# Kernel tuning notes

Hardware: AMD Instinct MI355X
Metric: run time of the kernel (lower is better)

The kernel has to match this reference:

```python
import jax, jax.numpy as jnp
import numpy as np

N_NODES = 100000
N_EDGES = 3200000
PERIODS = 12
C_IN, C_OUT, F_OUT = 1, 4, 12


def setup_inputs() -> dict:
    key = jax.random.key(0)
    ks = jax.random.split(key, 20)
    s = 0.1
    return {
        "x": jax.random.normal(ks[0], (N_NODES, C_IN, PERIODS), dtype=jnp.float32),
        "edge_index": jax.random.randint(ks[1], (2, N_EDGES), 0, N_NODES, dtype=jnp.int32),
        "conv_z_w": s * jax.random.normal(ks[2], (C_IN, C_OUT), dtype=jnp.float32),
        "conv_z_b": s * jax.random.normal(ks[3], (C_OUT,), dtype=jnp.float32),
        "lin_z_w": s * jax.random.normal(ks[4], (2 * C_OUT, C_OUT), dtype=jnp.float32),
        "lin_z_b": s * jax.random.normal(ks[5], (C_OUT,), dtype=jnp.float32),
        "conv_r_w": s * jax.random.normal(ks[6], (C_IN, C_OUT), dtype=jnp.float32),
        "conv_r_b": s * jax.random.normal(ks[7], (C_OUT,), dtype=jnp.float32),
        "lin_r_w": s * jax.random.normal(ks[8], (2 * C_OUT, C_OUT), dtype=jnp.float32),
        "lin_r_b": s * jax.random.normal(ks[9], (C_OUT,), dtype=jnp.float32),
        "conv_h_w": s * jax.random.normal(ks[10], (C_IN, C_OUT), dtype=jnp.float32),
        "conv_h_b": s * jax.random.normal(ks[11], (C_OUT,), dtype=jnp.float32),
        "lin_h_w": s * jax.random.normal(ks[12], (2 * C_OUT, C_OUT), dtype=jnp.float32),
        "lin_h_b": s * jax.random.normal(ks[13], (C_OUT,), dtype=jnp.float32),
        "att": jax.random.normal(ks[14], (PERIODS,), dtype=jnp.float32),
        "out_w": s * jax.random.normal(ks[15], (C_OUT, F_OUT), dtype=jnp.float32),
        "out_b": s * jax.random.normal(ks[16], (F_OUT,), dtype=jnp.float32),
        "f": 12,
    }


def reference(x, edge_index, conv_z_w, conv_z_b, lin_z_w, lin_z_b,
              conv_r_w, conv_r_b, lin_r_w, lin_r_b,
              conv_h_w, conv_h_b, lin_h_w, lin_h_b,
              att, out_w, out_b, f):
    N, _, P = x.shape
    loops = jnp.arange(N, dtype=edge_index.dtype)
    src = jnp.concatenate([edge_index[0], loops])  # self loops, fill=1
    dst = jnp.concatenate([edge_index[1], loops])
    deg = jax.ops.segment_sum(jnp.ones_like(src, dtype=x.dtype), dst, num_segments=N)
    dinv = jnp.where(deg > 0, jax.lax.rsqrt(deg), 0.0)
    norm = dinv[src] * dinv[dst]  # [E+N] symmetric GCN normalization

    def gcn(xt, W, b):
        xw = xt @ W  # [N, C_OUT]
        msg = xw[src] * norm[:, None]
        return jax.ops.segment_sum(msg, dst, num_segments=N) + b

    H0 = jnp.zeros((N, conv_z_w.shape[1]), dtype=x.dtype)

    def tgcn_step(xt):  # xt: [N, C_IN]; A3TGCN does not carry H across periods
        z = jax.nn.sigmoid(jnp.concatenate([gcn(xt, conv_z_w, conv_z_b), H0], 1) @ lin_z_w + lin_z_b)
        r = jax.nn.sigmoid(jnp.concatenate([gcn(xt, conv_r_w, conv_r_b), H0], 1) @ lin_r_w + lin_r_b)
        h_t = jnp.tanh(jnp.concatenate([gcn(xt, conv_h_w, conv_h_b), r * H0], 1) @ lin_h_w + lin_h_b)
        return z * H0 + (1.0 - z) * h_t

    xs = jnp.transpose(x, (2, 0, 1))  # [P, N, C_IN]
    Hs = jax.vmap(tgcn_step)(xs)  # [P, N, C_OUT]
    probs = jax.nn.softmax(att)
    H_accum = jnp.einsum('p,pnd->nd', probs, Hs)  # attention over periods
    out = H_accum @ out_w + out_b  # [N, 12]
    return out[:, :f]
```

## Files before the change

### kernel.cpp

```cpp
#include <hip/hip_runtime.h>
#include <hip/hip_fp16.h>
#include <math.h>


#define PERIODS 12
#define BSZ     256
#define BSH     8
#define STRIDE  9216
#define SRCBITS 17
#define SMASK   ((1 << SRCBITS) - 1)
#define CH      8192
#define NT      1024
#define ACCW    7
#define BIAS_F  262144.f

struct Consts {
    float az[4], cz[4], ah[4], ch[4], probs[PERIODS];
};

typedef float vf2 __attribute__((ext_vector_type(2)));

__device__ __forceinline__ float dec1_manual(unsigned b) {
    unsigned e = (b >> 3) & 15u, m = b & 7u;
    float v = e ? __uint_as_float(((e + 120u) << 23) | (m << 20))
                : (float)m * 0.001953125f;
    return (b & 0x80u) ? -v : v;
}

__device__ __forceinline__ void dec4(unsigned u, float* o) {
#if __has_builtin(__builtin_amdgcn_cvt_pk_f32_fp8)
    vf2 lo = __builtin_amdgcn_cvt_pk_f32_fp8((int)u, false);
    vf2 hi = __builtin_amdgcn_cvt_pk_f32_fp8((int)u, true);
    o[0] = lo.x; o[1] = lo.y; o[2] = hi.x; o[3] = hi.y;
#else
    o[0] = dec1_manual(u & 255u);
    o[1] = dec1_manual((u >> 8) & 255u);
    o[2] = dec1_manual((u >> 16) & 255u);
    o[3] = dec1_manual(u >> 24);
#endif
}

__device__ __forceinline__ unsigned enc1_manual(float x) {
    unsigned s = (__float_as_uint(x) >> 24) & 0x80u;
    float a = fabsf(x);
    if (!(a > 0.f)) return s;
    a = fminf(a, 448.f);
    int eb = (int)(__float_as_uint(a) >> 23) - 127;
    int e = eb < -6 ? -6 : eb;
    float q = rintf(a * exp2f((float)(3 - e)));
    if (q >= 16.f) { e++; q = rintf(a * exp2f((float)(3 - e))); }
    if (e > 8) return s | 0x7Eu;
    int m = (int)q;
    unsigned ee, mm;
    if (m >= 8) { ee = (unsigned)(e + 7); mm = (unsigned)(m - 8); }
    else        { ee = 0u; mm = (unsigned)m; }
    return s | (ee << 3) | mm;
}

__device__ __forceinline__ unsigned pk4(float a, float b, float c, float d) {
#if __has_builtin(__builtin_amdgcn_cvt_pk_fp8_f32)
    int v = __builtin_amdgcn_cvt_pk_fp8_f32(a, b, 0, false);
    v = __builtin_amdgcn_cvt_pk_fp8_f32(c, d, v, true);
    return (unsigned)v;
#else
    return enc1_manual(a) | (enc1_manual(b) << 8) |
           (enc1_manual(c) << 16) | (enc1_manual(d) << 24);
#endif
}


__global__ __launch_bounds__(512) void k_setup(const float* conv_z_w, const float* conv_z_b,
                        const float* lin_z_w, const float* lin_z_b,
                        const float* conv_h_w, const float* conv_h_b,
                        const float* lin_h_w, const float* lin_h_b,
                        const float* att, Consts* C, int* gcur, int NB)
{
    int t = threadIdx.x;
    for (int i = t; i < NB; i += 512) gcur[i] = 0;
    if (t == 0) {
        for (int c = 0; c < 4; ++c) {
            float az = 0.f, cz = 0.f, ah = 0.f, ch = 0.f;
            for (int k = 0; k < 4; ++k) {
                az += conv_z_w[k] * lin_z_w[k * 4 + c];
                cz += conv_z_b[k] * lin_z_w[k * 4 + c];
                ah += conv_h_w[k] * lin_h_w[k * 4 + c];
                ch += conv_h_b[k] * lin_h_w[k * 4 + c];
            }
            C->az[c] = az; C->cz[c] = cz + lin_z_b[c];
            C->ah[c] = ah; C->ch[c] = ch + lin_h_b[c];
        }
        float m = att[0];
        for (int p = 1; p < PERIODS; ++p) m = fmaxf(m, att[p]);
        float e[PERIODS]; float s = 0.f;
        for (int p = 0; p < PERIODS; ++p) { e[p] = expf(att[p] - m); s += e[p]; }
        for (int p = 0; p < PERIODS; ++p) C->probs[p] = e[p] / s;
    }
}

__global__ __launch_bounds__(NT, 4) void k_binA(const int* __restrict__ ei,
                                                int* __restrict__ gcur,
                                                int* __restrict__ binned, int E) {
    __shared__ int hist[512];
    __shared__ int scn[512];
    __shared__ int gdel[512];
    __shared__ int sv[CH];
    __shared__ int sa[CH];
    int t = threadIdx.x;
    if (t < 512) hist[t] = 0;
    __syncthreads();
    int base = blockIdx.x * CH;
    int lim = min(E - base, CH);
    int rs[CH / NT], rd[CH / NT];
    #pragma unroll
    for (int k = 0; k < CH / NT; ++k) {
        int i = t + k * NT;
        if (i < lim) {
            rs[k] = ei[base + i];
            rd[k] = ei[E + base + i];
            atomicAdd(&hist[rd[k] >> BSH], 1);
        }
    }
    __syncthreads();
    int v = 0;
    if (t < 512) { v = hist[t]; scn[t] = v; }
    __syncthreads();
    for (int off = 1; off < 512; off <<= 1) {
        int tmp = 0;
        if (t < 512 && t >= off) tmp = scn[t - off];
        __syncthreads();
        if (t < 512) scn[t] += tmp;
        __syncthreads();
    }
    if (t < 512) {
        int excl = scn[t] - v;
        int g = (v > 0) ? atomicAdd(&gcur[t], v) : 0;
        gdel[t] = t * STRIDE + g - excl;
        hist[t] = excl;
    }
    __syncthreads();
    #pragma unroll
    for (int k = 0; k < CH / NT; ++k) {
        int i = t + k * NT;
        if (i < lim) {
            int s = rs[k];
            int d = rd[k];
            int b = d >> BSH;
            int pos = atomicAdd(&hist[b], 1);
            sv[pos] = ((d & (BSZ - 1)) << SRCBITS) | s;
            sa[pos] = gdel[b] + pos;
        }
    }
    __syncthreads();
    for (int j = t; j < lim; j += NT)
        binned[sa[j]] = sv[j];
}

__global__ __launch_bounds__(NT, 4) void k_degprep(const int* __restrict__ binned,
                                                   const int* __restrict__ gcur,
                                                   const float* __restrict__ x,
                                                   int* __restrict__ deg,
                                                   float* __restrict__ dinv,
                                                   uint4* __restrict__ xs8, int N) {
    __shared__ int hist[BSZ];
    int b = blockIdx.x, t = threadIdx.x;
    if (t < BSZ) hist[t] = 0;
    __syncthreads();
    int cnt = gcur[b];
    const int* bb = binned + b * STRIDE;
    for (int i = t; i < cnt; i += NT)
        atomicAdd(&hist[bb[i] >> SRCBITS], 1);
    __syncthreads();
    if (t >= BSZ) return;
    int n = (b << BSH) + t;
    if (n >= N) return;
    int dg = hist[t];
    deg[n] = dg;
    float di = rsqrtf((float)dg + 1.0f);
    dinv[n] = di;
    const float4* xv = (const float4*)(x + (size_t)n * PERIODS);
    float4 v0 = xv[0], v1 = xv[1], v2 = xv[2];
    uint4 r;
    r.x = pk4(v0.x * di, v0.y * di, v0.z * di, v0.w * di);
    r.y = pk4(v1.x * di, v1.y * di, v1.z * di, v1.w * di);
    r.z = pk4(v2.x * di, v2.y * di, v2.z * di, v2.w * di);
    r.w = 0;
    xs8[n] = r;
}

__device__ __forceinline__ void scat(unsigned long long* acc, int d, uint4 r) {
    float f[PERIODS];
    dec4(r.x, f + 0); dec4(r.y, f + 4); dec4(r.z, f + 8);
    int base = d * ACCW;
    #pragma unroll
    for (int k = 0; k < 6; ++k) {
        unsigned lo = (unsigned)__float2int_rn(fmaf(f[k],     512.f, BIAS_F));
        unsigned hi = (unsigned)__float2int_rn(fmaf(f[k + 6], 512.f, BIAS_F));
        atomicAdd(&acc[base + k], ((unsigned long long)hi << 32) | (unsigned long long)lo);
    }
}

__global__ __launch_bounds__(NT, 4) void k_agg(const int* __restrict__ binned,
                                               const int* __restrict__ gcur,
                                               const int* __restrict__ deg,
                                               const float* __restrict__ dinv,
                                               const uint4* __restrict__ xs8,
                                               const Consts* __restrict__ C,
                                               const float* __restrict__ out_w,
                                               const float* __restrict__ out_b,
                                               float* __restrict__ out, int N) {
    __shared__ unsigned long long acc[BSZ * ACCW];
    int b = blockIdx.x, t = threadIdx.x;
    for (int i = t; i < BSZ * ACCW; i += NT) acc[i] = 0ull;
    __syncthreads();
    int cnt = gcur[b];
    const int* bb = binned + b * STRIDE;
    int i = t;
    for (; i + 3 * NT < cnt; i += 4 * NT) {
        int p0 = bb[i];
        int p1 = bb[i + NT];
        int p2 = bb[i + 2 * NT];
        int p3 = bb[i + 3 * NT];
        uint4 r0 = xs8[p0 & SMASK];
        uint4 r1 = xs8[p1 & SMASK];
        uint4 r2 = xs8[p2 & SMASK];
        uint4 r3 = xs8[p3 & SMASK];
        scat(acc, p0 >> SRCBITS, r0);
        scat(acc, p1 >> SRCBITS, r1);
        scat(acc, p2 >> SRCBITS, r2);
        scat(acc, p3 >> SRCBITS, r3);
    }
    for (; i < cnt; i += NT) {
        int pv = bb[i];
        uint4 r = xs8[pv & SMASK];
        scat(acc, pv >> SRCBITS, r);
    }
    __syncthreads();

    if (t >= BSZ) return;
    int n = (b << BSH) + t;
    if (n >= N) return;

    int corr = deg[n] << 18;
    float a[PERIODS];
    {
        float f[PERIODS];
        uint4 r = xs8[n];
        dec4(r.x, f + 0); dec4(r.y, f + 4); dec4(r.z, f + 8);
        #pragma unroll
        for (int k = 0; k < 6; ++k) {
            unsigned long long u = acc[t * ACCW + k];
            int lo = (int)(unsigned)(u & 0xFFFFFFFFull) - corr;
            int hi = (int)(unsigned)(u >> 32) - corr;
            a[k]     = (float)lo * 0.001953125f + f[k];
            a[k + 6] = (float)hi * 0.001953125f + f[k + 6];
        }
    }

    float di = dinv[n];
    float hacc[4] = {0.f, 0.f, 0.f, 0.f};
    #pragma unroll
    for (int p = 0; p < PERIODS; ++p) {
        float ap = di * a[p];
        float pr = C->probs[p];
        #pragma unroll
        for (int c = 0; c < 4; ++c) {
            float zz = 1.f / (1.f + __expf(-(ap * C->az[c] + C->cz[c])));
            float hh = tanhf(ap * C->ah[c] + C->ch[c]);
            hacc[c] += pr * (1.f - zz) * hh;
        }
    }
    float o[PERIODS];
    #pragma unroll
    for (int f = 0; f < PERIODS; ++f) {
        float v = out_b[f];
        #pragma unroll
        for (int c = 0; c < 4; ++c) v += hacc[c] * out_w[c * PERIODS + f];
        o[f] = v;
    }
    float4* ov = (float4*)(out + (size_t)n * PERIODS);
    ov[0] = make_float4(o[0], o[1], o[2],  o[3]);
    ov[1] = make_float4(o[4], o[5], o[6],  o[7]);
    ov[2] = make_float4(o[8], o[9], o[10], o[11]);
}

extern "C" void kernel_launch(void* const* d_in, const int* in_sizes, int n_in,
                              void* d_out, int out_size, void* d_ws, size_t ws_size,
                              hipStream_t stream) {
    const float* x        = (const float*)d_in[0];
    const int*   ei       = (const int*)d_in[1];
    const float* conv_z_w = (const float*)d_in[2];
    const float* conv_z_b = (const float*)d_in[3];
    const float* lin_z_w  = (const float*)d_in[4];
    const float* lin_z_b  = (const float*)d_in[5];
    const float* conv_h_w = (const float*)d_in[10];
    const float* conv_h_b = (const float*)d_in[11];
    const float* lin_h_w  = (const float*)d_in[12];
    const float* lin_h_b  = (const float*)d_in[13];
    const float* att      = (const float*)d_in[14];
    const float* out_w    = (const float*)d_in[15];
    const float* out_b    = (const float*)d_in[16];
    float* out = (float*)d_out;

    const int N  = in_sizes[0] / PERIODS;
    const int E  = in_sizes[1] / 2;
    const int NB = (N + BSZ - 1) / BSZ;
    const int gA = (E + CH - 1) / CH;

    char* ws = (char*)d_ws;
    size_t off = 0;
    Consts* consts = (Consts*)(ws + off);  off += (sizeof(Consts) + 255) & ~255ull;
    int*    gcur   = (int*)(ws + off);     off += ((size_t)NB * 4 + 255) & ~255ull;
    int*    deg    = (int*)(ws + off);     off += ((size_t)N * 4 + 255) & ~255ull;
    float*  dinv   = (float*)(ws + off);   off += ((size_t)N * 4 + 255) & ~255ull;
    uint4*  xs8    = (uint4*)(ws + off);   off += ((size_t)(N + 256) * 16 + 255) & ~255ull;
    int*    binned = (int*)(ws + off);     off += ((size_t)NB * STRIDE * 4 + 255) & ~255ull;
    (void)ws_size; (void)n_in; (void)out_size;

    k_setup<<<1, 512, 0, stream>>>(conv_z_w, conv_z_b, lin_z_w, lin_z_b,
                                   conv_h_w, conv_h_b, lin_h_w, lin_h_b, att,
                                   consts, gcur, NB);
    k_binA<<<gA, NT, 0, stream>>>(ei, gcur, binned, E);
    k_degprep<<<NB, NT, 0, stream>>>(binned, gcur, x, deg, dinv, xs8, N);
    k_agg<<<NB, NT, 0, stream>>>(binned, gcur, deg, dinv, xs8, consts,
                                 out_w, out_b, out, N);
}
```

Measured before the change: 160.0 us.

## Split per-bin aggregation into sliced partial-accumulate kernel plus merge kernel

```diff
diff --git a/kernel.cpp b/kernel.cpp
--- a/kernel.cpp
+++ b/kernel.cpp
@@ -6,7 +6,9 @@
 #define PERIODS 12
 #define BSZ     256
 #define BSH     8
-#define STRIDE  9216
+#define STRIDE  13312
+#define SLICE   3328
+#define NSLICE  4
 #define SRCBITS 17
 #define SMASK   ((1 << SRCBITS) - 1)
 #define CH      8192
@@ -99,7 +101,7 @@
 
 __global__ __launch_bounds__(NT, 4) void k_binA(const int* __restrict__ ei,
                                                 int* __restrict__ gcur,
-                                                int* __restrict__ binned, int E) {
+                                                int* __restrict__ binned, int E, int N) {
     __shared__ int hist[512];
     __shared__ int scn[512];
     __shared__ int gdel[512];
@@ -131,10 +133,13 @@
         if (t < 512) scn[t] += tmp;
         __syncthreads();
     }
+    int gbase = 0, vp = 0;
     if (t < 512) {
         int excl = scn[t] - v;
-        int g = (v > 0) ? atomicAdd(&gcur[t], v) : 0;
-        gdel[t] = t * STRIDE + g - excl;
+        vp = (v + 15) & ~15;
+        int g = (vp > 0) ? atomicAdd(&gcur[t], vp) : 0;
+        gbase = t * STRIDE + g;
+        gdel[t] = gbase - excl;
         hist[t] = excl;
     }
     __syncthreads();
@@ -153,6 +158,10 @@
     __syncthreads();
     for (int j = t; j < lim; j += NT)
         binned[sa[j]] = sv[j];
+    if (t < 512) {
+        for (int j = v; j < vp; ++j)
+            binned[gbase + j] = N;
+    }
 }
 
 __global__ __launch_bounds__(NT, 4) void k_degprep(const int* __restrict__ binned,
@@ -167,9 +176,12 @@
     __syncthreads();
     int cnt = gcur[b];
     const int* bb = binned + b * STRIDE;
-    for (int i = t; i < cnt; i += NT)
-        atomicAdd(&hist[bb[i] >> SRCBITS], 1);
-    __syncthreads();
+    for (int i = t; i < cnt; i += NT) {
+        int pv = bb[i];
+        if ((pv & SMASK) < N) atomicAdd(&hist[pv >> SRCBITS], 1);
+    }
+    __syncthreads();
+    if (b == 0 && t == 0) xs8[N] = make_uint4(0, 0, 0, 0);
     if (t >= BSZ) return;
     int n = (b << BSH) + t;
     if (n >= N) return;
@@ -199,8 +211,44 @@
     }
 }
 
-__global__ __launch_bounds__(NT, 4) void k_agg(const int* __restrict__ binned,
-                                               const int* __restrict__ gcur,
+__global__ __launch_bounds__(512) void k_aggp(const int* __restrict__ binned,
+                                              const int* __restrict__ gcur,
+                                              const uint4* __restrict__ xs8,
+                                              unsigned long long* __restrict__ pacc,
+                                              int N) {
+    __shared__ unsigned long long acc[BSZ * ACCW];
+    int b = blockIdx.x >> 2, s = blockIdx.x & 3;
+    int t = threadIdx.x;
+    for (int i = t; i < BSZ * ACCW; i += 512) acc[i] = 0ull;
+    __syncthreads();
+    int cnt = gcur[b];
+    int end = min(cnt, (s + 1) * SLICE);
+    const int* bb = binned + b * STRIDE;
+    int i = s * SLICE + t;
+    for (; i + 512 < end; i += 1024) {
+        int p0 = bb[i];
+        int p1 = bb[i + 512];
+        int s0 = p0 & SMASK, s1 = p1 & SMASK;
+        uint4 r0 = xs8[s0];
+        uint4 r1 = xs8[s1];
+        if (s0 < N) scat(acc, p0 >> SRCBITS, r0);
+        if (s1 < N) scat(acc, p1 >> SRCBITS, r1);
+    }
+    for (; i < end; i += 512) {
+        int pv = bb[i];
+        int sv = pv & SMASK;
+        uint4 r = xs8[sv];
+        if (sv < N) scat(acc, pv >> SRCBITS, r);
+    }
+    __syncthreads();
+    unsigned long long* pb = pacc + (size_t)(b * NSLICE + s) * (BSZ * 6);
+    for (int j = t; j < BSZ * 6; j += 512) {
+        int node = j / 6, k = j - node * 6;
+        pb[j] = acc[node * ACCW + k];
+    }
+}
+
+__global__ __launch_bounds__(256) void k_merge(const unsigned long long* __restrict__ pacc,
                                                const int* __restrict__ deg,
                                                const float* __restrict__ dinv,
                                                const uint4* __restrict__ xs8,
@@ -208,37 +256,17 @@
                                                const float* __restrict__ out_w,
                                                const float* __restrict__ out_b,
                                                float* __restrict__ out, int N) {
-    __shared__ unsigned long long acc[BSZ * ACCW];
     int b = blockIdx.x, t = threadIdx.x;
-    for (int i = t; i < BSZ * ACCW; i += NT) acc[i] = 0ull;
-    __syncthreads();
-    int cnt = gcur[b];
-    const int* bb = binned + b * STRIDE;
-    int i = t;
-    for (; i + 3 * NT < cnt; i += 4 * NT) {
-        int p0 = bb[i];
-        int p1 = bb[i + NT];
-        int p2 = bb[i + 2 * NT];
-        int p3 = bb[i + 3 * NT];
-        uint4 r0 = xs8[p0 & SMASK];
-        uint4 r1 = xs8[p1 & SMASK];
-        uint4 r2 = xs8[p2 & SMASK];
-        uint4 r3 = xs8[p3 & SMASK];
-        scat(acc, p0 >> SRCBITS, r0);
-        scat(acc, p1 >> SRCBITS, r1);
-        scat(acc, p2 >> SRCBITS, r2);
-        scat(acc, p3 >> SRCBITS, r3);
-    }
-    for (; i < cnt; i += NT) {
-        int pv = bb[i];
-        uint4 r = xs8[pv & SMASK];
-        scat(acc, pv >> SRCBITS, r);
-    }
-    __syncthreads();
-
-    if (t >= BSZ) return;
     int n = (b << BSH) + t;
     if (n >= N) return;
+
+    unsigned long long sum[6] = {0ull, 0ull, 0ull, 0ull, 0ull, 0ull};
+    const unsigned long long* pb = pacc + (size_t)b * NSLICE * (BSZ * 6) + t * 6;
+    #pragma unroll
+    for (int s = 0; s < NSLICE; ++s) {
+        #pragma unroll
+        for (int k = 0; k < 6; ++k) sum[k] += pb[s * (BSZ * 6) + k];
+    }
 
     int corr = deg[n] << 18;
     float a[PERIODS];
@@ -248,9 +276,8 @@
         dec4(r.x, f + 0); dec4(r.y, f + 4); dec4(r.z, f + 8);
         #pragma unroll
         for (int k = 0; k < 6; ++k) {
-            unsigned long long u = acc[t * ACCW + k];
-            int lo = (int)(unsigned)(u & 0xFFFFFFFFull) - corr;
-            int hi = (int)(unsigned)(u >> 32) - corr;
+            int lo = (int)(unsigned)(sum[k] & 0xFFFFFFFFull) - corr;
+            int hi = (int)(unsigned)(sum[k] >> 32) - corr;
             a[k]     = (float)lo * 0.001953125f + f[k];
             a[k + 6] = (float)hi * 0.001953125f + f[k + 6];
         }
@@ -314,13 +341,16 @@
     float*  dinv   = (float*)(ws + off);   off += ((size_t)N * 4 + 255) & ~255ull;
     uint4*  xs8    = (uint4*)(ws + off);   off += ((size_t)(N + 256) * 16 + 255) & ~255ull;
     int*    binned = (int*)(ws + off);     off += ((size_t)NB * STRIDE * 4 + 255) & ~255ull;
+    unsigned long long* pacc = (unsigned long long*)(ws + off);
+    off += ((size_t)NB * NSLICE * BSZ * 6 * 8 + 255) & ~255ull;
     (void)ws_size; (void)n_in; (void)out_size;
 
     k_setup<<<1, 512, 0, stream>>>(conv_z_w, conv_z_b, lin_z_w, lin_z_b,
                                    conv_h_w, conv_h_b, lin_h_w, lin_h_b, att,
                                    consts, gcur, NB);
-    k_binA<<<gA, NT, 0, stream>>>(ei, gcur, binned, E);
+    k_binA<<<gA, NT, 0, stream>>>(ei, gcur, binned, E, N);
     k_degprep<<<NB, NT, 0, stream>>>(binned, gcur, x, deg, dinv, xs8, N);
-    k_agg<<<NB, NT, 0, stream>>>(binned, gcur, deg, dinv, xs8, consts,
-                                 out_w, out_b, out, N);
-}
+    k_aggp<<<NB * NSLICE, 512, 0, stream>>>(binned, gcur, xs8, pacc, N);
+    k_merge<<<NB, 256, 0, stream>>>(pacc, deg, dinv, xs8, consts,
+                                    out_w, out_b, out, N);
+}
```

Result: no change. 163.2 us (+2.0%).

## Replicate shared accumulators 4x, pad bins to 16, fold setup into aggregation

Applied to the files above, without the earlier changes.

```diff
diff --git a/kernel.cpp b/kernel.cpp
--- a/kernel.cpp
+++ b/kernel.cpp
@@ -6,17 +6,14 @@
 #define PERIODS 12
 #define BSZ     256
 #define BSH     8
-#define STRIDE  9216
+#define STRIDE  13312
 #define SRCBITS 17
 #define SMASK   ((1 << SRCBITS) - 1)
 #define CH      8192
 #define NT      1024
 #define ACCW    7
+#define ACPY    1799
 #define BIAS_F  262144.f
-
-struct Consts {
-    float az[4], cz[4], ah[4], ch[4], probs[PERIODS];
-};
 
 typedef float vf2 __attribute__((ext_vector_type(2)));
 
@@ -69,37 +66,9 @@
 }
 
 
-__global__ __launch_bounds__(512) void k_setup(const float* conv_z_w, const float* conv_z_b,
-                        const float* lin_z_w, const float* lin_z_b,
-                        const float* conv_h_w, const float* conv_h_b,
-                        const float* lin_h_w, const float* lin_h_b,
-                        const float* att, Consts* C, int* gcur, int NB)
-{
-    int t = threadIdx.x;
-    for (int i = t; i < NB; i += 512) gcur[i] = 0;
-    if (t == 0) {
-        for (int c = 0; c < 4; ++c) {
-            float az = 0.f, cz = 0.f, ah = 0.f, ch = 0.f;
-            for (int k = 0; k < 4; ++k) {
-                az += conv_z_w[k] * lin_z_w[k * 4 + c];
-                cz += conv_z_b[k] * lin_z_w[k * 4 + c];
-                ah += conv_h_w[k] * lin_h_w[k * 4 + c];
-                ch += conv_h_b[k] * lin_h_w[k * 4 + c];
-            }
-            C->az[c] = az; C->cz[c] = cz + lin_z_b[c];
-            C->ah[c] = ah; C->ch[c] = ch + lin_h_b[c];
-        }
-        float m = att[0];
-        for (int p = 1; p < PERIODS; ++p) m = fmaxf(m, att[p]);
-        float e[PERIODS]; float s = 0.f;
-        for (int p = 0; p < PERIODS; ++p) { e[p] = expf(att[p] - m); s += e[p]; }
-        for (int p = 0; p < PERIODS; ++p) C->probs[p] = e[p] / s;
-    }
-}
-
 __global__ __launch_bounds__(NT, 4) void k_binA(const int* __restrict__ ei,
                                                 int* __restrict__ gcur,
-                                                int* __restrict__ binned, int E) {
+                                                int* __restrict__ binned, int E, int N) {
     __shared__ int hist[512];
     __shared__ int scn[512];
     __shared__ int gdel[512];
@@ -131,10 +100,13 @@
         if (t < 512) scn[t] += tmp;
         __syncthreads();
     }
+    int gbase = 0, vp = 0;
     if (t < 512) {
         int excl = scn[t] - v;
-        int g = (v > 0) ? atomicAdd(&gcur[t], v) : 0;
-        gdel[t] = t * STRIDE + g - excl;
+        vp = (v + 15) & ~15;
+        int g = (vp > 0) ? atomicAdd(&gcur[t], vp) : 0;
+        gbase = t * STRIDE + g;
+        gdel[t] = gbase - excl;
         hist[t] = excl;
     }
     __syncthreads();
@@ -153,6 +125,10 @@
     __syncthreads();
     for (int j = t; j < lim; j += NT)
         binned[sa[j]] = sv[j];
+    if (t < 512) {
+        for (int j = v; j < vp; ++j)
+            binned[gbase + j] = N;
+    }
 }
 
 __global__ __launch_bounds__(NT, 4) void k_degprep(const int* __restrict__ binned,
@@ -161,19 +137,23 @@
                                                    int* __restrict__ deg,
                                                    float* __restrict__ dinv,
                                                    uint4* __restrict__ xs8, int N) {
-    __shared__ int hist[BSZ];
+    __shared__ int hist[4 * 257];
     int b = blockIdx.x, t = threadIdx.x;
-    if (t < BSZ) hist[t] = 0;
+    for (int i = t; i < 4 * 257; i += NT) hist[i] = 0;
     __syncthreads();
     int cnt = gcur[b];
     const int* bb = binned + b * STRIDE;
-    for (int i = t; i < cnt; i += NT)
-        atomicAdd(&hist[bb[i] >> SRCBITS], 1);
-    __syncthreads();
+    int cpy = (t & 3) * 257;
+    for (int i = t; i < cnt; i += NT) {
+        int pv = bb[i];
+        if ((pv & SMASK) < N) atomicAdd(&hist[cpy + (pv >> SRCBITS)], 1);
+    }
+    __syncthreads();
+    if (b == 0 && t == 0) xs8[N] = make_uint4(0, 0, 0, 0);
     if (t >= BSZ) return;
     int n = (b << BSH) + t;
     if (n >= N) return;
-    int dg = hist[t];
+    int dg = hist[t] + hist[257 + t] + hist[514 + t] + hist[771 + t];
     deg[n] = dg;
     float di = rsqrtf((float)dg + 1.0f);
     dinv[n] = di;
@@ -187,31 +167,40 @@
     xs8[n] = r;
 }
 
-__device__ __forceinline__ void scat(unsigned long long* acc, int d, uint4 r) {
+__device__ __forceinline__ void scat(unsigned long long* accb, int d, uint4 r) {
     float f[PERIODS];
     dec4(r.x, f + 0); dec4(r.y, f + 4); dec4(r.z, f + 8);
-    int base = d * ACCW;
+    int ba = d * ACCW;
     #pragma unroll
     for (int k = 0; k < 6; ++k) {
         unsigned lo = (unsigned)__float2int_rn(fmaf(f[k],     512.f, BIAS_F));
         unsigned hi = (unsigned)__float2int_rn(fmaf(f[k + 6], 512.f, BIAS_F));
-        atomicAdd(&acc[base + k], ((unsigned long long)hi << 32) | (unsigned long long)lo);
-    }
-}
-
-__global__ __launch_bounds__(NT, 4) void k_agg(const int* __restrict__ binned,
+        atomicAdd(&accb[ba + k], ((unsigned long long)hi << 32) | (unsigned long long)lo);
+    }
+}
+
+__global__ __launch_bounds__(NT, 2) void k_agg(const int* __restrict__ binned,
                                                const int* __restrict__ gcur,
                                                const int* __restrict__ deg,
                                                const float* __restrict__ dinv,
                                                const uint4* __restrict__ xs8,
-                                               const Consts* __restrict__ C,
+                                               const float* __restrict__ conv_z_w,
+                                               const float* __restrict__ conv_z_b,
+                                               const float* __restrict__ lin_z_w,
+                                               const float* __restrict__ lin_z_b,
+                                               const float* __restrict__ conv_h_w,
+                                               const float* __restrict__ conv_h_b,
+                                               const float* __restrict__ lin_h_w,
+                                               const float* __restrict__ lin_h_b,
+                                               const float* __restrict__ att,
                                                const float* __restrict__ out_w,
                                                const float* __restrict__ out_b,
                                                float* __restrict__ out, int N) {
-    __shared__ unsigned long long acc[BSZ * ACCW];
+    __shared__ unsigned long long acc[4 * ACPY];
     int b = blockIdx.x, t = threadIdx.x;
-    for (int i = t; i < BSZ * ACCW; i += NT) acc[i] = 0ull;
-    __syncthreads();
+    for (int i = t; i < 4 * ACPY; i += NT) acc[i] = 0ull;
+    __syncthreads();
+    unsigned long long* accb = acc + (t & 3) * ACPY;
     int cnt = gcur[b];
     const int* bb = binned + b * STRIDE;
     int i = t;
@@ -220,25 +209,54 @@
         int p1 = bb[i + NT];
         int p2 = bb[i + 2 * NT];
         int p3 = bb[i + 3 * NT];
-        uint4 r0 = xs8[p0 & SMASK];
-        uint4 r1 = xs8[p1 & SMASK];
-        uint4 r2 = xs8[p2 & SMASK];
-        uint4 r3 = xs8[p3 & SMASK];
-        scat(acc, p0 >> SRCBITS, r0);
-        scat(acc, p1 >> SRCBITS, r1);
-        scat(acc, p2 >> SRCBITS, r2);
-        scat(acc, p3 >> SRCBITS, r3);
+        int s0 = p0 & SMASK, s1 = p1 & SMASK, s2 = p2 & SMASK, s3 = p3 & SMASK;
+        uint4 r0 = xs8[s0];
+        uint4 r1 = xs8[s1];
+        uint4 r2 = xs8[s2];
+        uint4 r3 = xs8[s3];
+        if (s0 < N) scat(accb, p0 >> SRCBITS, r0);
+        if (s1 < N) scat(accb, p1 >> SRCBITS, r1);
+        if (s2 < N) scat(accb, p2 >> SRCBITS, r2);
+        if (s3 < N) scat(accb, p3 >> SRCBITS, r3);
     }
     for (; i < cnt; i += NT) {
         int pv = bb[i];
-        uint4 r = xs8[pv & SMASK];
-        scat(acc, pv >> SRCBITS, r);
+        int sv = pv & SMASK;
+        uint4 r = xs8[sv];
+        if (sv < N) scat(accb, pv >> SRCBITS, r);
     }
     __syncthreads();
 
     if (t >= BSZ) return;
     int n = (b << BSH) + t;
     if (n >= N) return;
+
+    float az[4], cz[4], ah[4], ch[4];
+    #pragma unroll
+    for (int c = 0; c < 4; ++c) {
+        float a1 = 0.f, c1 = 0.f, a2 = 0.f, c2 = 0.f;
+        #pragma unroll
+        for (int k = 0; k < 4; ++k) {
+            a1 += conv_z_w[k] * lin_z_w[k * 4 + c];
+            c1 += conv_z_b[k] * lin_z_w[k * 4 + c];
+            a2 += conv_h_w[k] * lin_h_w[k * 4 + c];
+            c2 += conv_h_b[k] * lin_h_w[k * 4 + c];
+        }
+        az[c] = a1; cz[c] = c1 + lin_z_b[c];
+        ah[c] = a2; ch[c] = c2 + lin_h_b[c];
+    }
+    float probs[PERIODS];
+    {
+        float m = att[0];
+        #pragma unroll
+        for (int p = 1; p < PERIODS; ++p) m = fmaxf(m, att[p]);
+        float ssum = 0.f;
+        #pragma unroll
+        for (int p = 0; p < PERIODS; ++p) { probs[p] = expf(att[p] - m); ssum += probs[p]; }
+        float inv = 1.f / ssum;
+        #pragma unroll
+        for (int p = 0; p < PERIODS; ++p) probs[p] *= inv;
+    }
 
     int corr = deg[n] << 18;
     float a[PERIODS];
@@ -246,9 +264,11 @@
         float f[PERIODS];
         uint4 r = xs8[n];
         dec4(r.x, f + 0); dec4(r.y, f + 4); dec4(r.z, f + 8);
+        int ba = t * ACCW;
         #pragma unroll
         for (int k = 0; k < 6; ++k) {
-            unsigned long long u = acc[t * ACCW + k];
+            unsigned long long u = acc[ba + k] + acc[ACPY + ba + k]
+                                 + acc[2 * ACPY + ba + k] + acc[3 * ACPY + ba + k];
             int lo = (int)(unsigned)(u & 0xFFFFFFFFull) - corr;
             int hi = (int)(unsigned)(u >> 32) - corr;
             a[k]     = (float)lo * 0.001953125f + f[k];
@@ -261,11 +281,11 @@
     #pragma unroll
     for (int p = 0; p < PERIODS; ++p) {
         float ap = di * a[p];
-        float pr = C->probs[p];
+        float pr = probs[p];
         #pragma unroll
         for (int c = 0; c < 4; ++c) {
-            float zz = 1.f / (1.f + __expf(-(ap * C->az[c] + C->cz[c])));
-            float hh = tanhf(ap * C->ah[c] + C->ch[c]);
+            float zz = 1.f / (1.f + __expf(-(ap * az[c] + cz[c])));
+            float hh = tanhf(ap * ah[c] + ch[c]);
             hacc[c] += pr * (1.f - zz) * hh;
         }
     }
@@ -308,7 +328,6 @@
 
     char* ws = (char*)d_ws;
     size_t off = 0;
-    Consts* consts = (Consts*)(ws + off);  off += (sizeof(Consts) + 255) & ~255ull;
     int*    gcur   = (int*)(ws + off);     off += ((size_t)NB * 4 + 255) & ~255ull;
     int*    deg    = (int*)(ws + off);     off += ((size_t)N * 4 + 255) & ~255ull;
     float*  dinv   = (float*)(ws + off);   off += ((size_t)N * 4 + 255) & ~255ull;
@@ -316,11 +335,11 @@
     int*    binned = (int*)(ws + off);     off += ((size_t)NB * STRIDE * 4 + 255) & ~255ull;
     (void)ws_size; (void)n_in; (void)out_size;
 
-    k_setup<<<1, 512, 0, stream>>>(conv_z_w, conv_z_b, lin_z_w, lin_z_b,
-                                   conv_h_w, conv_h_b, lin_h_w, lin_h_b, att,
-                                   consts, gcur, NB);
-    k_binA<<<gA, NT, 0, stream>>>(ei, gcur, binned, E);
+    hipMemsetAsync(gcur, 0, (size_t)NB * 4, stream);
+    k_binA<<<gA, NT, 0, stream>>>(ei, gcur, binned, E, N);
     k_degprep<<<NB, NT, 0, stream>>>(binned, gcur, x, deg, dinv, xs8, N);
-    k_agg<<<NB, NT, 0, stream>>>(binned, gcur, deg, dinv, xs8, consts,
-                                 out_w, out_b, out, N);
-}
+    k_agg<<<NB, NT, 0, stream>>>(binned, gcur, deg, dinv, xs8,
+                                 conv_z_w, conv_z_b, lin_z_w, lin_z_b,
+                                 conv_h_w, conv_h_b, lin_h_w, lin_h_b,
+                                 att, out_w, out_b, out, N);
+}
```

Measured after the change: 168.5 us. 1.05x slower.

## Drop setup kernel, compute constants per-thread, shrink binning blocks

Applied to the files above, without the earlier changes.

```diff
diff --git a/kernel.cpp b/kernel.cpp
--- a/kernel.cpp
+++ b/kernel.cpp
@@ -6,17 +6,14 @@
 #define PERIODS 12
 #define BSZ     256
 #define BSH     8
-#define STRIDE  9216
+#define STRIDE  13312
 #define SRCBITS 17
 #define SMASK   ((1 << SRCBITS) - 1)
-#define CH      8192
+#define CH      4096
+#define NTB     512
 #define NT      1024
 #define ACCW    7
 #define BIAS_F  262144.f
-
-struct Consts {
-    float az[4], cz[4], ah[4], ch[4], probs[PERIODS];
-};
 
 typedef float vf2 __attribute__((ext_vector_type(2)));
 
@@ -69,51 +66,23 @@
 }
 
 
-__global__ __launch_bounds__(512) void k_setup(const float* conv_z_w, const float* conv_z_b,
-                        const float* lin_z_w, const float* lin_z_b,
-                        const float* conv_h_w, const float* conv_h_b,
-                        const float* lin_h_w, const float* lin_h_b,
-                        const float* att, Consts* C, int* gcur, int NB)
-{
-    int t = threadIdx.x;
-    for (int i = t; i < NB; i += 512) gcur[i] = 0;
-    if (t == 0) {
-        for (int c = 0; c < 4; ++c) {
-            float az = 0.f, cz = 0.f, ah = 0.f, ch = 0.f;
-            for (int k = 0; k < 4; ++k) {
-                az += conv_z_w[k] * lin_z_w[k * 4 + c];
-                cz += conv_z_b[k] * lin_z_w[k * 4 + c];
-                ah += conv_h_w[k] * lin_h_w[k * 4 + c];
-                ch += conv_h_b[k] * lin_h_w[k * 4 + c];
-            }
-            C->az[c] = az; C->cz[c] = cz + lin_z_b[c];
-            C->ah[c] = ah; C->ch[c] = ch + lin_h_b[c];
-        }
-        float m = att[0];
-        for (int p = 1; p < PERIODS; ++p) m = fmaxf(m, att[p]);
-        float e[PERIODS]; float s = 0.f;
-        for (int p = 0; p < PERIODS; ++p) { e[p] = expf(att[p] - m); s += e[p]; }
-        for (int p = 0; p < PERIODS; ++p) C->probs[p] = e[p] / s;
-    }
-}
-
-__global__ __launch_bounds__(NT, 4) void k_binA(const int* __restrict__ ei,
-                                                int* __restrict__ gcur,
-                                                int* __restrict__ binned, int E) {
+__global__ __launch_bounds__(NTB) void k_binA(const int* __restrict__ ei,
+                                              int* __restrict__ gcur,
+                                              int* __restrict__ binned, int E) {
     __shared__ int hist[512];
     __shared__ int scn[512];
     __shared__ int gdel[512];
     __shared__ int sv[CH];
     __shared__ int sa[CH];
     int t = threadIdx.x;
-    if (t < 512) hist[t] = 0;
+    hist[t] = 0;
     __syncthreads();
     int base = blockIdx.x * CH;
     int lim = min(E - base, CH);
-    int rs[CH / NT], rd[CH / NT];
-    #pragma unroll
-    for (int k = 0; k < CH / NT; ++k) {
-        int i = t + k * NT;
+    int rs[CH / NTB], rd[CH / NTB];
+    #pragma unroll
+    for (int k = 0; k < CH / NTB; ++k) {
+        int i = t + k * NTB;
         if (i < lim) {
             rs[k] = ei[base + i];
             rd[k] = ei[E + base + i];
@@ -121,26 +90,23 @@
         }
     }
     __syncthreads();
-    int v = 0;
-    if (t < 512) { v = hist[t]; scn[t] = v; }
+    int v = hist[t];
+    scn[t] = v;
     __syncthreads();
     for (int off = 1; off < 512; off <<= 1) {
-        int tmp = 0;
-        if (t < 512 && t >= off) tmp = scn[t - off];
+        int tmp = (t >= off) ? scn[t - off] : 0;
         __syncthreads();
-        if (t < 512) scn[t] += tmp;
+        scn[t] += tmp;
         __syncthreads();
     }
-    if (t < 512) {
-        int excl = scn[t] - v;
-        int g = (v > 0) ? atomicAdd(&gcur[t], v) : 0;
-        gdel[t] = t * STRIDE + g - excl;
-        hist[t] = excl;
-    }
-    __syncthreads();
-    #pragma unroll
-    for (int k = 0; k < CH / NT; ++k) {
-        int i = t + k * NT;
+    int excl = scn[t] - v;
+    int g = (v > 0) ? atomicAdd(&gcur[t], v) : 0;
+    gdel[t] = t * STRIDE + g - excl;
+    hist[t] = excl;
+    __syncthreads();
+    #pragma unroll
+    for (int k = 0; k < CH / NTB; ++k) {
+        int i = t + k * NTB;
         if (i < lim) {
             int s = rs[k];
             int d = rd[k];
@@ -151,7 +117,7 @@
         }
     }
     __syncthreads();
-    for (int j = t; j < lim; j += NT)
+    for (int j = t; j < lim; j += NTB)
         binned[sa[j]] = sv[j];
 }
 
@@ -204,7 +170,15 @@
                                                const int* __restrict__ deg,
                                                const float* __restrict__ dinv,
                                                const uint4* __restrict__ xs8,
-                                               const Consts* __restrict__ C,
+                                               const float* __restrict__ conv_z_w,
+                                               const float* __restrict__ conv_z_b,
+                                               const float* __restrict__ lin_z_w,
+                                               const float* __restrict__ lin_z_b,
+                                               const float* __restrict__ conv_h_w,
+                                               const float* __restrict__ conv_h_b,
+                                               const float* __restrict__ lin_h_w,
+                                               const float* __restrict__ lin_h_b,
+                                               const float* __restrict__ att,
                                                const float* __restrict__ out_w,
                                                const float* __restrict__ out_b,
                                                float* __restrict__ out, int N) {
@@ -240,15 +214,43 @@
     int n = (b << BSH) + t;
     if (n >= N) return;
 
+    float az[4], cz[4], ah[4], chh[4];
+    #pragma unroll
+    for (int c = 0; c < 4; ++c) {
+        float a1 = 0.f, c1 = 0.f, a2 = 0.f, c2 = 0.f;
+        #pragma unroll
+        for (int k = 0; k < 4; ++k) {
+            a1 += conv_z_w[k] * lin_z_w[k * 4 + c];
+            c1 += conv_z_b[k] * lin_z_w[k * 4 + c];
+            a2 += conv_h_w[k] * lin_h_w[k * 4 + c];
+            c2 += conv_h_b[k] * lin_h_w[k * 4 + c];
+        }
+        az[c] = a1; cz[c] = c1 + lin_z_b[c];
+        ah[c] = a2; chh[c] = c2 + lin_h_b[c];
+    }
+    float probs[PERIODS];
+    {
+        float m = att[0];
+        #pragma unroll
+        for (int p = 1; p < PERIODS; ++p) m = fmaxf(m, att[p]);
+        float ssum = 0.f;
+        #pragma unroll
+        for (int p = 0; p < PERIODS; ++p) { probs[p] = expf(att[p] - m); ssum += probs[p]; }
+        float inv = 1.f / ssum;
+        #pragma unroll
+        for (int p = 0; p < PERIODS; ++p) probs[p] *= inv;
+    }
+
     int corr = deg[n] << 18;
     float a[PERIODS];
     {
         float f[PERIODS];
         uint4 r = xs8[n];
         dec4(r.x, f + 0); dec4(r.y, f + 4); dec4(r.z, f + 8);
+        int ba = t * ACCW;
         #pragma unroll
         for (int k = 0; k < 6; ++k) {
-            unsigned long long u = acc[t * ACCW + k];
+            unsigned long long u = acc[ba + k];
             int lo = (int)(unsigned)(u & 0xFFFFFFFFull) - corr;
             int hi = (int)(unsigned)(u >> 32) - corr;
             a[k]     = (float)lo * 0.001953125f + f[k];
@@ -261,11 +263,11 @@
     #pragma unroll
     for (int p = 0; p < PERIODS; ++p) {
         float ap = di * a[p];
-        float pr = C->probs[p];
+        float pr = probs[p];
         #pragma unroll
         for (int c = 0; c < 4; ++c) {
-            float zz = 1.f / (1.f + __expf(-(ap * C->az[c] + C->cz[c])));
-            float hh = tanhf(ap * C->ah[c] + C->ch[c]);
+            float zz = 1.f / (1.f + __expf(-(ap * az[c] + cz[c])));
+            float hh = tanhf(ap * ah[c] + chh[c]);
             hacc[c] += pr * (1.f - zz) * hh;
         }
     }
@@ -308,19 +310,18 @@
 
     char* ws = (char*)d_ws;
     size_t off = 0;
-    Consts* consts = (Consts*)(ws + off);  off += (sizeof(Consts) + 255) & ~255ull;
-    int*    gcur   = (int*)(ws + off);     off += ((size_t)NB * 4 + 255) & ~255ull;
+    int*    gcur   = (int*)(ws + off);     off += ((size_t)512 * 4 + 255) & ~255ull;
     int*    deg    = (int*)(ws + off);     off += ((size_t)N * 4 + 255) & ~255ull;
     float*  dinv   = (float*)(ws + off);   off += ((size_t)N * 4 + 255) & ~255ull;
     uint4*  xs8    = (uint4*)(ws + off);   off += ((size_t)(N + 256) * 16 + 255) & ~255ull;
     int*    binned = (int*)(ws + off);     off += ((size_t)NB * STRIDE * 4 + 255) & ~255ull;
     (void)ws_size; (void)n_in; (void)out_size;
 
-    k_setup<<<1, 512, 0, stream>>>(conv_z_w, conv_z_b, lin_z_w, lin_z_b,
-                                   conv_h_w, conv_h_b, lin_h_w, lin_h_b, att,
-                                   consts, gcur, NB);
-    k_binA<<<gA, NT, 0, stream>>>(ei, gcur, binned, E);
+    hipMemsetAsync(gcur, 0, (size_t)512 * 4, stream);
+    k_binA<<<gA, NTB, 0, stream>>>(ei, gcur, binned, E);
     k_degprep<<<NB, NT, 0, stream>>>(binned, gcur, x, deg, dinv, xs8, N);
-    k_agg<<<NB, NT, 0, stream>>>(binned, gcur, deg, dinv, xs8, consts,
-                                 out_w, out_b, out, N);
-}
+    k_agg<<<NB, NT, 0, stream>>>(binned, gcur, deg, dinv, xs8,
+                                 conv_z_w, conv_z_b, lin_z_w, lin_z_b,
+                                 conv_h_w, conv_h_b, lin_h_w, lin_h_b,
+                                 att, out_w, out_b, out, N);
+}
```

New measurement: 170.6 us. +6.6%, slower.
